# Kernel tuning notes

Measured on AMD Instinct MI355X. Metric: run time of the kernel, lower is better.

The kernel has to match this reference:

```python
import jax, jax.numpy as jnp
import numpy as np

B, S, H, I = 2, 2048, 4096, 11008  # batch, seq, hidden_size, intermediate_size (Llama-7B)


def setup_inputs() -> dict:
    key = jax.random.key(0)
    ks = jax.random.split(key, 11)
    # int8 activations and weights (SmoothQuant W8A8)
    hidden_states = jax.random.randint(ks[0], (B, S, H), -128, 128, dtype=jnp.int8)
    w_gate = jax.random.randint(ks[1], (I, H), -128, 128, dtype=jnp.int8)
    w_up = jax.random.randint(ks[2], (I, H), -128, 128, dtype=jnp.int8)
    w_down = jax.random.randint(ks[3], (H, I), -128, 128, dtype=jnp.int8)
    # dequant scales (alpha = input_scale * weight_scale), small positive
    gate_a = jax.random.uniform(ks[4], (1,), dtype=jnp.float32) * 1e-4 + 1e-5
    up_a = jax.random.uniform(ks[5], (1,), dtype=jnp.float32) * 1e-4 + 1e-5
    down_a = jax.random.uniform(ks[6], (1,), dtype=jnp.float32) * 1e-4 + 1e-5
    # fp32 biases
    gate_b = jax.random.normal(ks[7], (I,), dtype=jnp.float32) * 0.01
    up_b = jax.random.normal(ks[8], (I,), dtype=jnp.float32) * 0.01
    down_b = jax.random.normal(ks[9], (H,), dtype=jnp.float32) * 0.01
    # requantization scale for down_proj input
    down_scale = jax.random.uniform(ks[10], (1,), dtype=jnp.float32) * 0.05 + 0.01
    return {
        "hidden_states": hidden_states,
        "w_gate": w_gate, "w_up": w_up, "w_down": w_down,
        "gate_a": gate_a, "gate_b": gate_b,
        "up_a": up_a, "up_b": up_b,
        "down_a": down_a, "down_b": down_b,
        "down_scale": down_scale,
    }


def _i8_gemm(x_i8, w_i8):
    return jnp.einsum("bsk,nk->bsn", x_i8, w_i8, preferred_element_type=jnp.int32)


def reference(hidden_states, w_gate, w_up, w_down,
              gate_a, gate_b, up_a, up_b, down_a, down_b, down_scale):
    # gate_proj: W8A8 GEMM -> dequant (alpha) + fp32 bias -> fused SiLU
    g = _i8_gemm(hidden_states, w_gate).astype(jnp.float32) * gate_a[0] + gate_b
    gate_out = g * jax.nn.sigmoid(g)  # SiLU
    # up_proj: W8A8 GEMM -> dequant + fp32 bias
    up_out = _i8_gemm(hidden_states, w_up).astype(jnp.float32) * up_a[0] + up_b
    inter = gate_out * up_out
    # requantize to int8 for down_proj input
    q = jnp.clip(jnp.round(inter / down_scale[0]), -128, 127).astype(jnp.int8)
    # down_proj: W8A8 GEMM -> dequant + fp32 bias
    down_out = _i8_gemm(q, w_down).astype(jnp.float32) * down_a[0] + down_b
    return down_out  # [B, S, H] fp32
```

## Files before the change

### kernel.cpp

```cpp
#include <hip/hip_runtime.h>
#include <cstdint>


typedef int v4i  __attribute__((ext_vector_type(4)));
typedef int v16i __attribute__((ext_vector_type(16)));

typedef const void __attribute__((address_space(1)))* gas_ptr;
typedef void __attribute__((address_space(3)))* las_ptr;

static constexpr int M_TOT = 4096;
static constexpr int HDIM  = 4096;
static constexpr int IDIM  = 11008;

#define BM 128
#define BN 128
#define BK 128

__device__ __forceinline__ void pack16(const int* __restrict__ src,
                                       int8_t* __restrict__ dst, int t) {
  const int4* s = (const int4*)(src) + t * 4;
  int4 v0 = s[0], v1 = s[1], v2 = s[2], v3 = s[3];
  int p0 = (v0.x & 0xff) | ((v0.y & 0xff) << 8) | ((v0.z & 0xff) << 16) | (v0.w << 24);
  int p1 = (v1.x & 0xff) | ((v1.y & 0xff) << 8) | ((v1.z & 0xff) << 16) | (v1.w << 24);
  int p2 = (v2.x & 0xff) | ((v2.y & 0xff) << 8) | ((v2.z & 0xff) << 16) | (v2.w << 24);
  int p3 = (v3.x & 0xff) | ((v3.y & 0xff) << 8) | ((v3.z & 0xff) << 16) | (v3.w << 24);
  ((int4*)dst)[t] = make_int4(p0, p1, p2, p3);
}

static constexpr int CX = (M_TOT * HDIM) / 16;
static constexpr int CW = (IDIM * HDIM) / 16;
static constexpr int CTOT = CX + 3 * CW;

__global__ __launch_bounds__(256) void k_pack_all(
    const int* __restrict__ X32, const int* __restrict__ Wg32,
    const int* __restrict__ Wu32, const int* __restrict__ Wd32,
    int8_t* __restrict__ Xp, int8_t* __restrict__ Wgp,
    int8_t* __restrict__ Wup, int8_t* __restrict__ Wdp) {
  int t = blockIdx.x * blockDim.x + threadIdx.x;
  if (t >= CTOT) return;
  if (t < CX)               { pack16(X32,  Xp,  t); return; }
  t -= CX;
  if (t < CW)               { pack16(Wg32, Wgp, t); return; }
  t -= CW;
  if (t < CW)               { pack16(Wu32, Wup, t); return; }
  t -= CW;
  pack16(Wd32, Wdp, t);
}

__device__ __forceinline__ void async_stage_16kb(const int8_t* __restrict__ gbase,
                                                 int ld, int8_t* lds, int tid) {
#pragma unroll
  for (int it = 0; it < 4; ++it) {
    const int chunk = it * 256 + tid;
    const int row   = chunk >> 3;
    const int slot  = chunk & 7;
    const int gch   = slot ^ (row & 7);
    const int8_t* g = gbase + row * ld + gch * 16;
    int8_t* l = lds + chunk * 16;
    __builtin_amdgcn_global_load_lds((gas_ptr)g, (las_ptr)l, 16, 0, 0);
  }
}

__device__ __forceinline__ v4i frag_ld(const int8_t* lds, int row, int kc, int half) {
  const int ch  = kc + half;
  const int sch = ch ^ (row & 7);
  return *(const v4i*)(lds + row * 128 + sch * 16);
}

#define MFMA_I8(a, b, c) __builtin_amdgcn_mfma_i32_32x32x32_i8((a), (b), (c), 0, 0, 0)

__global__ __launch_bounds__(256, 2) void k_gateup(
    const int8_t* __restrict__ X,
    const int8_t* __restrict__ Wg,
    const int8_t* __restrict__ Wu,
    const float* __restrict__ gate_a, const float* __restrict__ gate_b,
    const float* __restrict__ up_a,   const float* __restrict__ up_b,
    const float* __restrict__ down_scale,
    int8_t* __restrict__ Q) {
  __shared__ __align__(16) int8_t sA[BM * BK];
  __shared__ __align__(16) int8_t sG[BN * BK];
  __shared__ __align__(16) int8_t sU[BN * BK];

  const int tid  = threadIdx.x;
  const int lane = tid & 63;
  const int wave = tid >> 6;
  const int wm   = wave >> 1;
  const int wn   = wave & 1;
  const int half = lane >> 5;
  const int ln31 = lane & 31;

  const int m0 = blockIdx.x * BM;
  const int n0 = blockIdx.y * BN;

  const int8_t* Ab = X  + (size_t)m0 * HDIM;
  const int8_t* Gb = Wg + (size_t)n0 * HDIM;
  const int8_t* Ub = Wu + (size_t)n0 * HDIM;

  v16i accG[2][2], accU[2][2];
#pragma unroll
  for (int i = 0; i < 2; ++i)
#pragma unroll
    for (int j = 0; j < 2; ++j)
#pragma unroll
      for (int e = 0; e < 16; ++e) { accG[i][j][e] = 0; accU[i][j][e] = 0; }

  const int rA = wm * 64 + ln31;
  const int rB = wn * 64 + ln31;

  for (int k0 = 0; k0 < HDIM; k0 += BK) {
    async_stage_16kb(Ab + k0, HDIM, sA, tid);
    async_stage_16kb(Gb + k0, HDIM, sG, tid);
    async_stage_16kb(Ub + k0, HDIM, sU, tid);
    __syncthreads();
#pragma unroll
    for (int kc = 0; kc < 8; kc += 2) {
      v4i a0 = frag_ld(sA, rA,      kc, half);
      v4i a1 = frag_ld(sA, rA + 32, kc, half);
      v4i g0 = frag_ld(sG, rB,      kc, half);
      v4i g1 = frag_ld(sG, rB + 32, kc, half);
      v4i u0 = frag_ld(sU, rB,      kc, half);
      v4i u1 = frag_ld(sU, rB + 32, kc, half);
      accG[0][0] = MFMA_I8(a0, g0, accG[0][0]);
      accG[0][1] = MFMA_I8(a0, g1, accG[0][1]);
      accG[1][0] = MFMA_I8(a1, g0, accG[1][0]);
      accG[1][1] = MFMA_I8(a1, g1, accG[1][1]);
      accU[0][0] = MFMA_I8(a0, u0, accU[0][0]);
      accU[0][1] = MFMA_I8(a0, u1, accU[0][1]);
      accU[1][0] = MFMA_I8(a1, u0, accU[1][0]);
      accU[1][1] = MFMA_I8(a1, u1, accU[1][1]);
    }
    __syncthreads();
  }

  const float ga = gate_a[0];
  const float ua = up_a[0];
  const float inv_ds = 1.0f / down_scale[0];

#pragma unroll
  for (int tm = 0; tm < 2; ++tm) {
#pragma unroll
    for (int tn = 0; tn < 2; ++tn) {
      const int n = n0 + wn * 64 + tn * 32 + ln31;
      const float gb = gate_b[n];
      const float ub = up_b[n];
#pragma unroll
      for (int r = 0; r < 16; ++r) {
        const int row_l = (r & 3) + 8 * (r >> 2) + 4 * half;
        const int m = m0 + wm * 64 + tm * 32 + row_l;
        const float g = (float)accG[tm][tn][r] * ga + gb;
        const float u = (float)accU[tm][tn][r] * ua + ub;
        const float sg = g / (1.0f + __expf(-g));
        const float inter = sg * u;
        float qf = rintf(inter * inv_ds);
        qf = fminf(127.0f, fmaxf(-128.0f, qf));
        Q[(size_t)m * IDIM + n] = (int8_t)qf;
      }
    }
  }
}

__global__ __launch_bounds__(256, 2) void k_down(
    const int8_t* __restrict__ Q,
    const int8_t* __restrict__ Wd,
    const float* __restrict__ down_a, const float* __restrict__ down_b,
    float* __restrict__ Out) {
  __shared__ __align__(16) int8_t sA[256 * BK];
  __shared__ __align__(16) int8_t sB[128 * BK];

  const int tid  = threadIdx.x;
  const int lane = tid & 63;
  const int wave = tid >> 6;
  const int wm   = wave >> 1;
  const int wn   = wave & 1;
  const int half = lane >> 5;
  const int ln31 = lane & 31;

  const int m0 = blockIdx.x * 256;
  const int n0 = blockIdx.y * 128;

  const int8_t* Ab = Q  + (size_t)m0 * IDIM;
  const int8_t* Bb = Wd + (size_t)n0 * IDIM;

  v16i acc[4][2];
#pragma unroll
  for (int i = 0; i < 4; ++i)
#pragma unroll
    for (int j = 0; j < 2; ++j)
#pragma unroll
      for (int e = 0; e < 16; ++e) acc[i][j][e] = 0;

  const int rA = wm * 128 + ln31;
  const int rB = wn * 64 + ln31;

  for (int k0 = 0; k0 < IDIM; k0 += BK) {
    async_stage_16kb(Ab + k0, IDIM, sA, tid);
    async_stage_16kb(Ab + (size_t)128 * IDIM + k0, IDIM, sA + 128 * BK, tid);
    async_stage_16kb(Bb + k0, IDIM, sB, tid);
    __syncthreads();
#pragma unroll
    for (int kc = 0; kc < 8; kc += 2) {
      v4i a0 = frag_ld(sA, rA,      kc, half);
      v4i a1 = frag_ld(sA, rA + 32, kc, half);
      v4i a2 = frag_ld(sA, rA + 64, kc, half);
      v4i a3 = frag_ld(sA, rA + 96, kc, half);
      v4i b0 = frag_ld(sB, rB,      kc, half);
      v4i b1 = frag_ld(sB, rB + 32, kc, half);
      acc[0][0] = MFMA_I8(a0, b0, acc[0][0]);
      acc[0][1] = MFMA_I8(a0, b1, acc[0][1]);
      acc[1][0] = MFMA_I8(a1, b0, acc[1][0]);
      acc[1][1] = MFMA_I8(a1, b1, acc[1][1]);
      acc[2][0] = MFMA_I8(a2, b0, acc[2][0]);
      acc[2][1] = MFMA_I8(a2, b1, acc[2][1]);
      acc[3][0] = MFMA_I8(a3, b0, acc[3][0]);
      acc[3][1] = MFMA_I8(a3, b1, acc[3][1]);
    }
    __syncthreads();
  }

  const float da = down_a[0];
#pragma unroll
  for (int tm = 0; tm < 4; ++tm) {
#pragma unroll
    for (int tn = 0; tn < 2; ++tn) {
      const int n = n0 + wn * 64 + tn * 32 + ln31;
      const float db = down_b[n];
#pragma unroll
      for (int r = 0; r < 16; ++r) {
        const int row_l = (r & 3) + 8 * (r >> 2) + 4 * half;
        const int m = m0 + wm * 128 + tm * 32 + row_l;
        Out[(size_t)m * HDIM + n] = (float)acc[tm][tn][r] * da + db;
      }
    }
  }
}

extern "C" void kernel_launch(void* const* d_in, const int* in_sizes, int n_in,
                              void* d_out, int out_size, void* d_ws, size_t ws_size,
                              hipStream_t stream) {
  const int* X32        = (const int*)d_in[0];
  const int* Wg32       = (const int*)d_in[1];
  const int* Wu32       = (const int*)d_in[2];
  const int* Wd32       = (const int*)d_in[3];
  const float* gate_a   = (const float*)d_in[4];
  const float* gate_b   = (const float*)d_in[5];
  const float* up_a     = (const float*)d_in[6];
  const float* up_b     = (const float*)d_in[7];
  const float* down_a   = (const float*)d_in[8];
  const float* down_b   = (const float*)d_in[9];
  const float* down_scale = (const float*)d_in[10];
  float* Out = (float*)d_out;

  const size_t nX = (size_t)M_TOT * HDIM;
  const size_t nW = (size_t)IDIM * HDIM;

  int8_t* Q   = (int8_t*)d_ws;
  int8_t* Xp  = Q   + nW;
  int8_t* Wgp = Xp  + nX;
  int8_t* Wup = Wgp + nW;
  int8_t* Wdp = Wup + nW;

  k_pack_all<<<(CTOT + 255) / 256, 256, 0, stream>>>(X32, Wg32, Wu32, Wd32,
                                                     Xp, Wgp, Wup, Wdp);

  dim3 g1(M_TOT / BM, IDIM / BN);
  k_gateup<<<g1, dim3(256), 0, stream>>>(Xp, Wgp, Wup, gate_a, gate_b, up_a, up_b,
                                         down_scale, Q);
  dim3 g2(M_TOT / 256, HDIM / 128);
  k_down<<<g2, dim3(256), 0, stream>>>(Q, Wdp, down_a, down_b, Out);
}
```

Before: 1.110 ms.

## Triple-buffer LDS with BK=64 async prefetch pipeline in both GEMMs

Both GEMM kernels switch from a single-buffered BK=128 load-then-compute loop to a three-stage ring of BK=64 LDS buffers. Global-to-LDS loads run two tiles ahead, synchronised with explicit vmcnt waits and a single barrier per iteration. The change also uses a new paired-row swizzle, reassigns waves (gate/up waves split only along N; down now uses 128x256 tiles) and raises wave priority around the MFMA block. The aim is to hide global load latency behind matrix work. The cost is 72KB of LDS per block, which may limit occupancy to two blocks per CU, and more complex wait-count bookkeeping.

```diff
diff --git a/kernel.cpp b/kernel.cpp
--- a/kernel.cpp
+++ b/kernel.cpp
@@ -12,9 +12,27 @@
 static constexpr int HDIM  = 4096;
 static constexpr int IDIM  = 11008;
 
-#define BM 128
-#define BN 128
-#define BK 128
+#define MFMA_I8(a, b, c) __builtin_amdgcn_mfma_i32_32x32x32_i8((a), (b), (c), 0, 0, 0)
+#define BAR()        asm volatile("s_barrier" ::: "memory")
+#define WAIT_VM(N)   asm volatile("s_waitcnt vmcnt(" #N ")" ::: "memory")
+#define SETPRIO(P)   __builtin_amdgcn_s_setprio(P)
+
+__device__ __forceinline__ void gload16(const int8_t* g, int8_t* l) {
+  __builtin_amdgcn_global_load_lds((gas_ptr)g, (las_ptr)l, 16, 0, 0);
+}
+
+__device__ __forceinline__ v4i frag64(const int8_t* lds, int row, int c) {
+  const int pair = row >> 1;
+  const int slot = ((c << 1) | (row & 1)) ^ (pair & 7);
+  return *(const v4i*)(lds + pair * 128 + slot * 16);
+}
+
+__device__ __forceinline__ void relmap64(int rel, int& row, int& col) {
+  const int pair = rel >> 3;
+  const int sl = (rel & 7) ^ (pair & 7);
+  row = 2 * pair + (sl & 1);
+  col = (sl >> 1) * 16;
+}
 
 __device__ __forceinline__ void pack16(const int* __restrict__ src,
                                        int8_t* __restrict__ dst, int t) {
@@ -47,28 +65,6 @@
   pack16(Wd32, Wdp, t);
 }
 
-__device__ __forceinline__ void async_stage_16kb(const int8_t* __restrict__ gbase,
-                                                 int ld, int8_t* lds, int tid) {
-#pragma unroll
-  for (int it = 0; it < 4; ++it) {
-    const int chunk = it * 256 + tid;
-    const int row   = chunk >> 3;
-    const int slot  = chunk & 7;
-    const int gch   = slot ^ (row & 7);
-    const int8_t* g = gbase + row * ld + gch * 16;
-    int8_t* l = lds + chunk * 16;
-    __builtin_amdgcn_global_load_lds((gas_ptr)g, (las_ptr)l, 16, 0, 0);
-  }
-}
-
-__device__ __forceinline__ v4i frag_ld(const int8_t* lds, int row, int kc, int half) {
-  const int ch  = kc + half;
-  const int sch = ch ^ (row & 7);
-  return *(const v4i*)(lds + row * 128 + sch * 16);
-}
-
-#define MFMA_I8(a, b, c) __builtin_amdgcn_mfma_i32_32x32x32_i8((a), (b), (c), 0, 0, 0)
-
 __global__ __launch_bounds__(256, 2) void k_gateup(
     const int8_t* __restrict__ X,
     const int8_t* __restrict__ Wg,
@@ -77,110 +73,157 @@
     const float* __restrict__ up_a,   const float* __restrict__ up_b,
     const float* __restrict__ down_scale,
     int8_t* __restrict__ Q) {
-  __shared__ __align__(16) int8_t sA[BM * BK];
-  __shared__ __align__(16) int8_t sG[BN * BK];
-  __shared__ __align__(16) int8_t sU[BN * BK];
+  __shared__ __align__(16) int8_t lds8[3 * 24576];
 
   const int tid  = threadIdx.x;
   const int lane = tid & 63;
   const int wave = tid >> 6;
-  const int wm   = wave >> 1;
-  const int wn   = wave & 1;
+  const int wn   = wave;
   const int half = lane >> 5;
   const int ln31 = lane & 31;
 
-  const int m0 = blockIdx.x * BM;
-  const int n0 = blockIdx.y * BN;
+  const int m0 = blockIdx.x * 128;
+  const int n0 = blockIdx.y * 128;
 
   const int8_t* Ab = X  + (size_t)m0 * HDIM;
   const int8_t* Gb = Wg + (size_t)n0 * HDIM;
   const int8_t* Ub = Wu + (size_t)n0 * HDIM;
 
-  v16i accG[2][2], accU[2][2];
-#pragma unroll
-  for (int i = 0; i < 2; ++i)
-#pragma unroll
-    for (int j = 0; j < 2; ++j)
-#pragma unroll
-      for (int e = 0; e < 16; ++e) { accG[i][j][e] = 0; accU[i][j][e] = 0; }
-
-  const int rA = wm * 64 + ln31;
-  const int rB = wn * 64 + ln31;
-
-  for (int k0 = 0; k0 < HDIM; k0 += BK) {
-    async_stage_16kb(Ab + k0, HDIM, sA, tid);
-    async_stage_16kb(Gb + k0, HDIM, sG, tid);
-    async_stage_16kb(Ub + k0, HDIM, sU, tid);
-    __syncthreads();
-#pragma unroll
-    for (int kc = 0; kc < 8; kc += 2) {
-      v4i a0 = frag_ld(sA, rA,      kc, half);
-      v4i a1 = frag_ld(sA, rA + 32, kc, half);
-      v4i g0 = frag_ld(sG, rB,      kc, half);
-      v4i g1 = frag_ld(sG, rB + 32, kc, half);
-      v4i u0 = frag_ld(sU, rB,      kc, half);
-      v4i u1 = frag_ld(sU, rB + 32, kc, half);
-      accG[0][0] = MFMA_I8(a0, g0, accG[0][0]);
-      accG[0][1] = MFMA_I8(a0, g1, accG[0][1]);
-      accG[1][0] = MFMA_I8(a1, g0, accG[1][0]);
-      accG[1][1] = MFMA_I8(a1, g1, accG[1][1]);
-      accU[0][0] = MFMA_I8(a0, u0, accU[0][0]);
-      accU[0][1] = MFMA_I8(a0, u1, accU[0][1]);
-      accU[1][0] = MFMA_I8(a1, u0, accU[1][0]);
-      accU[1][1] = MFMA_I8(a1, u1, accU[1][1]);
+  int r0, c0, r1, c1;
+  relmap64(tid,       r0, c0);
+  relmap64(tid + 256, r1, c1);
+  const size_t o0 = (size_t)r0 * HDIM + c0;
+  const size_t o1 = (size_t)r1 * HDIM + c1;
+  const int l0 = tid * 16;
+  const int l1 = (tid + 256) * 16;
+
+  v16i accG[4], accU[4];
+#pragma unroll
+  for (int i = 0; i < 4; ++i)
+#pragma unroll
+    for (int e = 0; e < 16; ++e) { accG[i][e] = 0; accU[i][e] = 0; }
+
+  const int rB = wn * 32 + ln31;
+
+#define GU_STAGE(rr, bb)                                        \
+  {                                                             \
+    int8_t* sb = &lds8[(bb) * 24576];                           \
+    const size_t ks = (size_t)(rr) * 64;                        \
+    gload16(Ab + ks + o0, sb + l0);                             \
+    gload16(Ab + ks + o1, sb + l1);                             \
+    gload16(Gb + ks + o0, sb + 8192 + l0);                      \
+    gload16(Gb + ks + o1, sb + 8192 + l1);                      \
+    gload16(Ub + ks + o0, sb + 16384 + l0);                     \
+    gload16(Ub + ks + o1, sb + 16384 + l1);                     \
+  }
+
+  GU_STAGE(0, 0)
+  GU_STAGE(1, 1)
+  WAIT_VM(6);
+  BAR();
+
+  const int NT = HDIM / 64;
+  int bc = 0;
+  int bs = 2;
+  for (int r = 0; r < NT; ++r) {
+    if (r + 2 < NT) GU_STAGE(r + 2, bs)
+
+    const int8_t* bufA = &lds8[bc * 24576];
+    const int8_t* bufG = bufA + 8192;
+    const int8_t* bufU = bufA + 16384;
+    SETPRIO(1);
+#pragma unroll
+    for (int ks = 0; ks < 2; ++ks) {
+      const int c = 2 * ks + half;
+      v4i a0 = frag64(bufA, ln31,      c);
+      v4i a1 = frag64(bufA, ln31 + 32, c);
+      v4i a2 = frag64(bufA, ln31 + 64, c);
+      v4i a3 = frag64(bufA, ln31 + 96, c);
+      v4i gg = frag64(bufG, rB, c);
+      v4i uu = frag64(bufU, rB, c);
+      accG[0] = MFMA_I8(a0, gg, accG[0]);
+      accU[0] = MFMA_I8(a0, uu, accU[0]);
+      accG[1] = MFMA_I8(a1, gg, accG[1]);
+      accU[1] = MFMA_I8(a1, uu, accU[1]);
+      accG[2] = MFMA_I8(a2, gg, accG[2]);
+      accU[2] = MFMA_I8(a2, uu, accU[2]);
+      accG[3] = MFMA_I8(a3, gg, accG[3]);
+      accU[3] = MFMA_I8(a3, uu, accU[3]);
     }
-    __syncthreads();
-  }
+    SETPRIO(0);
+
+    if (r + 2 < NT)      { WAIT_VM(6); }
+    else if (r + 1 < NT) { WAIT_VM(0); }
+    if (r + 1 < NT) BAR();
+
+    bc = (bc == 2) ? 0 : bc + 1;
+    bs = (bs == 2) ? 0 : bs + 1;
+  }
+#undef GU_STAGE
 
   const float ga = gate_a[0];
   const float ua = up_a[0];
   const float inv_ds = 1.0f / down_scale[0];
-
-#pragma unroll
-  for (int tm = 0; tm < 2; ++tm) {
-#pragma unroll
-    for (int tn = 0; tn < 2; ++tn) {
-      const int n = n0 + wn * 64 + tn * 32 + ln31;
-      const float gb = gate_b[n];
-      const float ub = up_b[n];
-#pragma unroll
-      for (int r = 0; r < 16; ++r) {
-        const int row_l = (r & 3) + 8 * (r >> 2) + 4 * half;
-        const int m = m0 + wm * 64 + tm * 32 + row_l;
-        const float g = (float)accG[tm][tn][r] * ga + gb;
-        const float u = (float)accU[tm][tn][r] * ua + ub;
-        const float sg = g / (1.0f + __expf(-g));
-        const float inter = sg * u;
-        float qf = rintf(inter * inv_ds);
-        qf = fminf(127.0f, fmaxf(-128.0f, qf));
-        Q[(size_t)m * IDIM + n] = (int8_t)qf;
-      }
+  const int n = n0 + wn * 32 + ln31;
+  const float gb = gate_b[n];
+  const float ub = up_b[n];
+
+#pragma unroll
+  for (int tm = 0; tm < 4; ++tm) {
+#pragma unroll
+    for (int r = 0; r < 16; ++r) {
+      const int row_l = (r & 3) + 8 * (r >> 2) + 4 * half;
+      const int m = m0 + tm * 32 + row_l;
+      const float g = (float)accG[tm][r] * ga + gb;
+      const float u = (float)accU[tm][r] * ua + ub;
+      const float sg = g / (1.0f + __expf(-g));
+      const float inter = sg * u;
+      float qf = rintf(inter * inv_ds);
+      qf = fminf(127.0f, fmaxf(-128.0f, qf));
+      Q[(size_t)m * IDIM + n] = (int8_t)qf;
     }
   }
 }
 
 __global__ __launch_bounds__(256, 2) void k_down(
-    const int8_t* __restrict__ Q,
+    const int8_t* __restrict__ Qm,
     const int8_t* __restrict__ Wd,
     const float* __restrict__ down_a, const float* __restrict__ down_b,
     float* __restrict__ Out) {
-  __shared__ __align__(16) int8_t sA[256 * BK];
-  __shared__ __align__(16) int8_t sB[128 * BK];
+  __shared__ __align__(16) int8_t lds8[3 * 24576];
 
   const int tid  = threadIdx.x;
   const int lane = tid & 63;
   const int wave = tid >> 6;
-  const int wm   = wave >> 1;
-  const int wn   = wave & 1;
+  const int wn   = wave;
   const int half = lane >> 5;
   const int ln31 = lane & 31;
 
-  const int m0 = blockIdx.x * 256;
-  const int n0 = blockIdx.y * 128;
-
-  const int8_t* Ab = Q  + (size_t)m0 * IDIM;
+  const int m0 = blockIdx.x * 128;
+  const int n0 = blockIdx.y * 256;
+
+  const int8_t* Ab = Qm + (size_t)m0 * IDIM;
   const int8_t* Bb = Wd + (size_t)n0 * IDIM;
 
+  int ra0, ca0, ra1, ca1;
+  relmap64(tid,       ra0, ca0);
+  relmap64(tid + 256, ra1, ca1);
+  const size_t oa0 = (size_t)ra0 * IDIM + ca0;
+  const size_t oa1 = (size_t)ra1 * IDIM + ca1;
+  int rb0, cb0, rb1, cb1, rb2, cb2, rb3, cb3;
+  relmap64(tid,       rb0, cb0);
+  relmap64(tid + 256, rb1, cb1);
+  relmap64(tid + 512, rb2, cb2);
+  relmap64(tid + 768, rb3, cb3);
+  const size_t ob0 = (size_t)rb0 * IDIM + cb0;
+  const size_t ob1 = (size_t)rb1 * IDIM + cb1;
+  const size_t ob2 = (size_t)rb2 * IDIM + cb2;
+  const size_t ob3 = (size_t)rb3 * IDIM + cb3;
+  const int l0 = tid * 16;
+  const int l1 = (tid + 256) * 16;
+  const int l2 = (tid + 512) * 16;
+  const int l3 = (tid + 768) * 16;
+
   v16i acc[4][2];
 #pragma unroll
   for (int i = 0; i < 4; ++i)
@@ -189,22 +232,43 @@
 #pragma unroll
       for (int e = 0; e < 16; ++e) acc[i][j][e] = 0;
 
-  const int rA = wm * 128 + ln31;
   const int rB = wn * 64 + ln31;
 
-  for (int k0 = 0; k0 < IDIM; k0 += BK) {
-    async_stage_16kb(Ab + k0, IDIM, sA, tid);
-    async_stage_16kb(Ab + (size_t)128 * IDIM + k0, IDIM, sA + 128 * BK, tid);
-    async_stage_16kb(Bb + k0, IDIM, sB, tid);
-    __syncthreads();
-#pragma unroll
-    for (int kc = 0; kc < 8; kc += 2) {
-      v4i a0 = frag_ld(sA, rA,      kc, half);
-      v4i a1 = frag_ld(sA, rA + 32, kc, half);
-      v4i a2 = frag_ld(sA, rA + 64, kc, half);
-      v4i a3 = frag_ld(sA, rA + 96, kc, half);
-      v4i b0 = frag_ld(sB, rB,      kc, half);
-      v4i b1 = frag_ld(sB, rB + 32, kc, half);
+#define DN_STAGE(rr, bb)                                        \
+  {                                                             \
+    int8_t* sb = &lds8[(bb) * 24576];                           \
+    const size_t ks = (size_t)(rr) * 64;                        \
+    gload16(Ab + ks + oa0, sb + l0);                            \
+    gload16(Ab + ks + oa1, sb + l1);                            \
+    gload16(Bb + ks + ob0, sb + 8192 + l0);                     \
+    gload16(Bb + ks + ob1, sb + 8192 + l1);                     \
+    gload16(Bb + ks + ob2, sb + 8192 + l2);                     \
+    gload16(Bb + ks + ob3, sb + 8192 + l3);                     \
+  }
+
+  DN_STAGE(0, 0)
+  DN_STAGE(1, 1)
+  WAIT_VM(6);
+  BAR();
+
+  const int NT = IDIM / 64;
+  int bc = 0;
+  int bs = 2;
+  for (int r = 0; r < NT; ++r) {
+    if (r + 2 < NT) DN_STAGE(r + 2, bs)
+
+    const int8_t* bufA = &lds8[bc * 24576];
+    const int8_t* bufB = bufA + 8192;
+    SETPRIO(1);
+#pragma unroll
+    for (int ks = 0; ks < 2; ++ks) {
+      const int c = 2 * ks + half;
+      v4i a0 = frag64(bufA, ln31,      c);
+      v4i a1 = frag64(bufA, ln31 + 32, c);
+      v4i a2 = frag64(bufA, ln31 + 64, c);
+      v4i a3 = frag64(bufA, ln31 + 96, c);
+      v4i b0 = frag64(bufB, rB,      c);
+      v4i b1 = frag64(bufB, rB + 32, c);
       acc[0][0] = MFMA_I8(a0, b0, acc[0][0]);
       acc[0][1] = MFMA_I8(a0, b1, acc[0][1]);
       acc[1][0] = MFMA_I8(a1, b0, acc[1][0]);
@@ -214,20 +278,28 @@
       acc[3][0] = MFMA_I8(a3, b0, acc[3][0]);
       acc[3][1] = MFMA_I8(a3, b1, acc[3][1]);
     }
-    __syncthreads();
-  }
+    SETPRIO(0);
+
+    if (r + 2 < NT)      { WAIT_VM(6); }
+    else if (r + 1 < NT) { WAIT_VM(0); }
+    if (r + 1 < NT) BAR();
+
+    bc = (bc == 2) ? 0 : bc + 1;
+    bs = (bs == 2) ? 0 : bs + 1;
+  }
+#undef DN_STAGE
 
   const float da = down_a[0];
 #pragma unroll
-  for (int tm = 0; tm < 4; ++tm) {
-#pragma unroll
-    for (int tn = 0; tn < 2; ++tn) {
-      const int n = n0 + wn * 64 + tn * 32 + ln31;
-      const float db = down_b[n];
+  for (int tn = 0; tn < 2; ++tn) {
+    const int n = n0 + wn * 64 + tn * 32 + ln31;
+    const float db = down_b[n];
+#pragma unroll
+    for (int tm = 0; tm < 4; ++tm) {
 #pragma unroll
       for (int r = 0; r < 16; ++r) {
         const int row_l = (r & 3) + 8 * (r >> 2) + 4 * half;
-        const int m = m0 + wm * 128 + tm * 32 + row_l;
+        const int m = m0 + tm * 32 + row_l;
         Out[(size_t)m * HDIM + n] = (float)acc[tm][tn][r] * da + db;
       }
     }
@@ -262,9 +334,9 @@
   k_pack_all<<<(CTOT + 255) / 256, 256, 0, stream>>>(X32, Wg32, Wu32, Wd32,
                                                      Xp, Wgp, Wup, Wdp);
 
-  dim3 g1(M_TOT / BM, IDIM / BN);
-  k_gateup<<<g1, dim3(256), 0, stream>>>(Xp, Wgp, Wup, gate_a, gate_b, up_a, up_b,
-                                         down_scale, Q);
-  dim3 g2(M_TOT / 256, HDIM / 128);
-  k_down<<<g2, dim3(256), 0, stream>>>(Q, Wdp, down_a, down_b, Out);
-}
+  k_gateup<<<dim3(M_TOT / 128, IDIM / 128), dim3(256), 0, stream>>>(
+      Xp, Wgp, Wup, gate_a, gate_b, up_a, up_b, down_scale, Q);
+
+  k_down<<<dim3(M_TOT / 128, HDIM / 256), dim3(256), 0, stream>>>(
+      Q, Wdp, down_a, down_b, Out);
+}
```

New measurement: 1.143 ms. 1.03x slower.
